# Performance work log

Measured on AMD Instinct MI355X. Metric: run time of the kernel, lower is better.

## Reference

```python
import jax, jax.numpy as jnp
import numpy as np

N_HEADS = 16
EMBED = 1024
HEAD_SIZE = 64
BLOCK = 2048
BATCH = 4


def setup_inputs() -> dict:
    key = jax.random.key(0)
    ks = jax.random.split(key, 6)
    s = 1.0 / np.sqrt(EMBED)
    X = jax.random.normal(ks[0], (BATCH, BLOCK, EMBED), dtype=jnp.float32)
    Wq = jax.random.normal(ks[1], (N_HEADS, EMBED, HEAD_SIZE), dtype=jnp.float32) * s
    Wk = jax.random.normal(ks[2], (N_HEADS, EMBED, HEAD_SIZE), dtype=jnp.float32) * s
    Wv = jax.random.normal(ks[3], (N_HEADS, EMBED, HEAD_SIZE), dtype=jnp.float32) * s
    Wo = jax.random.normal(ks[4], (EMBED, EMBED), dtype=jnp.float32) * s
    bo = jnp.zeros((EMBED,), dtype=jnp.float32)
    return {"X": X, "Wq": Wq, "Wk": Wk, "Wv": Wv, "Wo": Wo, "bo": bo}


def reference(X, Wq, Wk, Wv, Wo, bo):
    # X: [B, S, E]; Wq/Wk/Wv: [H, E, Dh]
    q = jnp.einsum("bse,hed->bhsd", X, Wq)
    k = jnp.einsum("bse,hed->bhsd", X, Wk)
    v = jnp.einsum("bse,hed->bhsd", X, Wv)
    scale = 1.0 / np.sqrt(HEAD_SIZE)
    scores = jnp.einsum("bhsd,bhtd->bhst", q, k) * scale  # [B,H,S,S]
    S = X.shape[1]
    causal = jnp.tril(jnp.ones((S, S), dtype=bool))
    scores = jnp.where(causal, scores, -jnp.inf)
    wei = jax.nn.softmax(scores, axis=-1)
    # dropout p=0.2 treated as identity (eval mode) for deterministic reference
    out = jnp.einsum("bhst,bhtd->bhsd", wei, v)  # [B,H,S,Dh]
    out = out.transpose(0, 2, 1, 3).reshape(X.shape[0], S, N_HEADS * HEAD_SIZE)
    return out @ Wo.T + bo
```

## Files before the change

kernel.cpp:

```cpp
#include <hip/hip_runtime.h>
#include <stdint.h>


typedef __bf16 bf16_t;
typedef __bf16 bf16x4 __attribute__((ext_vector_type(4)));
typedef __bf16 bf16x8 __attribute__((ext_vector_type(8)));
typedef float  f32x4  __attribute__((ext_vector_type(4)));
typedef float  f32x16 __attribute__((ext_vector_type(16)));
typedef unsigned int u32;

union V8 { bf16x8 v8; bf16x4 h[2]; u32 w[4]; };

__device__ __forceinline__ void gload_lds16(const void* g, void* l) {
  __builtin_amdgcn_global_load_lds((const __attribute__((address_space(1))) void*)g,
                                   (__attribute__((address_space(3))) void*)l, 16, 0, 0);
}


__global__ __launch_bounds__(256) void mha_prep_all(const float* __restrict__ X,
                                                    const float* __restrict__ Wq,
                                                    const float* __restrict__ Wk,
                                                    const float* __restrict__ Wv,
                                                    const float* __restrict__ Wo,
                                                    bf16_t* __restrict__ Xb,
                                                    bf16_t* __restrict__ Wob,
                                                    bf16_t* __restrict__ Wt) {
  const int bx = blockIdx.x;
  if (bx < 4608) {
    const float* src = (bx < 4096) ? X : Wo;
    bf16_t* dst = (bx < 4096) ? Xb : Wob;
    size_t base = (size_t)((bx < 4096) ? bx : bx - 4096) * 256 + threadIdx.x;
    size_t i = base * 8;
    const float4* p = (const float4*)(src + i);
    float4 a = p[0], b = p[1];
    bf16x8 o;
    o[0] = (__bf16)a.x; o[1] = (__bf16)a.y; o[2] = (__bf16)a.z; o[3] = (__bf16)a.w;
    o[4] = (__bf16)b.x; o[5] = (__bf16)b.y; o[6] = (__bf16)b.z; o[7] = (__bf16)b.w;
    *(bf16x8*)(dst + i) = o;
  } else {
    __shared__ float tile[64][65];
    const int pid = bx - 4608;
    const int e0 = (pid & 15) * 64;
    const int mh = pid >> 4;
    const int mat = mh >> 4, h = mh & 15;
    const float* W = (mat == 0) ? Wq : (mat == 1) ? Wk : Wv;
    const float sc = (mat == 0) ? 0.18033688011112042f : 1.0f;
    #pragma unroll
    for (int i = 0; i < 16; i++) {
      int idx = threadIdx.x + i * 256;
      int er = idx >> 6, d = idx & 63;
      tile[er][d] = W[(size_t)(h * 1024 + e0 + er) * 64 + d];
    }
    __syncthreads();
    #pragma unroll
    for (int i = 0; i < 16; i++) {
      int idx = threadIdx.x + i * 256;
      int dr = idx >> 6, ec = idx & 63;
      Wt[(size_t)(mat * 1024 + h * 64 + dr) * 1024 + e0 + ec] = (bf16_t)(tile[ec][dr] * sc);
    }
  }
}


__global__ __launch_bounds__(512, 2) void gemm192(const bf16_t* __restrict__ A,
                                                  const bf16_t* __restrict__ Bt,
                                                  bf16_t* __restrict__ C,
                                                  int M, int N, int K) {
  __shared__ __align__(16) char lds[131072];
  const int tid = threadIdx.x;
  const int l = tid & 63, w = tid >> 6;
  const int g = l >> 4, lg = l & 15;
  const int wr = w >> 2, wc = w & 3;
  const int bid = blockIdx.x;
  const int nbn = N / 192;
  const int gsw = (bid & 7) * (gridDim.x >> 3) + (bid >> 3);
  const long brow = (long)(gsw / nbn) * 256;
  const long bcol = (long)(gsw % nbn) * 192;

  f32x4 acc[8][3];
  #pragma unroll
  for (int im = 0; im < 8; im++)
    #pragma unroll
    for (int n = 0; n < 3; n++) acc[im][n] = (f32x4){0.f, 0.f, 0.f, 0.f};

  auto stage = [&](const bf16_t* base, long trow, int k0, int region, bool pad) {
    #pragma unroll
    for (int j = 0; j < 2; j++) {
      int p = (tid + j * 512) * 16;
      int row = p >> 6, slot = (p >> 4) & 3;
      int src = slot ^ ((row >> 1) & 3);
      int r2 = (pad && row >= 192) ? row - 192 : row;
      gload_lds16(base + (trow + r2) * (long)K + k0 + src * 8,
                  lds + region + p);
    }
  };

  stage(A,  brow, 0,  0,              false);
  stage(Bt, bcol, 0,  65536,          true);
  stage(A,  brow, 32, 16384,          false);
  stage(Bt, bcol, 32, 65536 + 16384,  true);
  stage(A,  brow, 64, 32768,          false);
  stage(Bt, bcol, 64, 65536 + 32768,  true);
  asm volatile("s_waitcnt vmcnt(4)" ::: "memory");
  __builtin_amdgcn_s_barrier();
  __builtin_amdgcn_sched_barrier(0);

  const int sw = (lg >> 1) & 3;
  const int nIter = K >> 7;
  for (int t = 0; t < nIter; t++) {
    const bool more = (t + 1 < nIter);
    const int kb = t * 128;
    #pragma unroll
    for (int ph = 0; ph < 8; ph++) {
      const int slot = ph >> 2;
      const int kh = (ph >> 1) & 1, mq = ph & 1;
      bf16x8 af[4], bfv[3];
      {
        const char* pA = lds + slot * 32768 + kh * 16384;
        const char* pB = pA + 65536;
        #pragma unroll
        for (int m = 0; m < 4; m++) {
          int wrow = wr * 128 + mq * 64 + m * 16 + lg;
          af[m] = *(const bf16x8*)(pA + wrow * 64 + ((g ^ sw) << 4));
        }
        #pragma unroll
        for (int n = 0; n < 3; n++) {
          int wrow = wc * 48 + n * 16 + lg;
          bfv[n] = *(const bf16x8*)(pB + wrow * 64 + ((g ^ sw) << 4));
        }
      }
      if (ph == 0)      stage(A,  brow, kb + 96,  32768 + 16384, false);
      else if (ph == 1) stage(Bt, bcol, kb + 96,  65536 + 32768 + 16384, true);
      else if (more) {
        if (ph == 2)      stage(A,  brow, kb + 128, 0, false);
        else if (ph == 3) stage(Bt, bcol, kb + 128, 65536, true);
        else if (ph == 4) stage(A,  brow, kb + 160, 16384, false);
        else if (ph == 5) stage(Bt, bcol, kb + 160, 65536 + 16384, true);
        else if (ph == 6) stage(A,  brow, kb + 192, 32768, false);
        else              stage(Bt, bcol, kb + 192, 65536 + 32768, true);
      }
      __builtin_amdgcn_s_barrier();
      asm volatile("s_waitcnt lgkmcnt(0)" ::: "memory");
      __builtin_amdgcn_sched_barrier(0);
      __builtin_amdgcn_s_setprio(1);
      #pragma unroll
      for (int m = 0; m < 4; m++)
        #pragma unroll
        for (int n = 0; n < 3; n++)
          acc[mq * 4 + m][n] =
              __builtin_amdgcn_mfma_f32_16x16x32_bf16(af[m], bfv[n], acc[mq * 4 + m][n], 0, 0, 0);
      __builtin_amdgcn_s_setprio(0);
      __builtin_amdgcn_sched_barrier(0);
      if (ph & 1) {
        if (more) asm volatile("s_waitcnt vmcnt(4)" ::: "memory");
        else if (ph == 1) asm volatile("s_waitcnt vmcnt(0)" ::: "memory");
      }
      __builtin_amdgcn_s_barrier();
      __builtin_amdgcn_sched_barrier(0);
    }
  }

  #pragma unroll
  for (int im = 0; im < 8; im++)
    #pragma unroll
    for (int n = 0; n < 3; n++) {
      long row0 = brow + wr * 128 + im * 16 + g * 4;
      long col  = bcol + wc * 48 + n * 16 + lg;
      #pragma unroll
      for (int r = 0; r < 4; r++)
        C[(row0 + r) * N + col] = (bf16_t)acc[im][n][r];
    }
}


template <int MODE>
__global__ __launch_bounds__(256) void gemm_bt(const bf16_t* __restrict__ A,
                                               const bf16_t* __restrict__ Bt,
                                               void* __restrict__ Cout,
                                               const float* __restrict__ bias,
                                               int M, int N, int K) {
  __shared__ bf16_t lA[128 * 32];
  __shared__ bf16_t lB[128 * 32];
  const int tid = threadIdx.x;
  const int l = tid & 63, w = tid >> 6;
  const int g = l >> 4, lg = l & 15;
  const int wr = w >> 1, wc = w & 1;
  const long brow = (long)blockIdx.y * 128;
  const long bcol = (long)blockIdx.x * 128;

  f32x4 acc[4][4];
  #pragma unroll
  for (int m = 0; m < 4; m++)
    #pragma unroll
    for (int n = 0; n < 4; n++) acc[m][n] = (f32x4){0.f, 0.f, 0.f, 0.f};

  const bf16_t* Ab = A + brow * K;
  const bf16_t* Bb = Bt + bcol * K;
  const int c0 = tid, c1 = tid + 256;
  const int r0 = c0 >> 2, o0 = (c0 & 3) * 8;
  const int r1 = c1 >> 2, o1 = (c1 & 3) * 8;

  for (int k0 = 0; k0 < K; k0 += 32) {
    __syncthreads();
    gload_lds16(Ab + (long)r0 * K + k0 + o0, lA + c0 * 8);
    gload_lds16(Ab + (long)r1 * K + k0 + o1, lA + c1 * 8);
    gload_lds16(Bb + (long)r0 * K + k0 + o0, lB + c0 * 8);
    gload_lds16(Bb + (long)r1 * K + k0 + o1, lB + c1 * 8);
    __syncthreads();
    bf16x8 af[4], bfr[4];
    #pragma unroll
    for (int m = 0; m < 4; m++)
      af[m] = *(const bf16x8*)(lA + (wr * 64 + m * 16 + lg) * 32 + g * 8);
    #pragma unroll
    for (int n = 0; n < 4; n++)
      bfr[n] = *(const bf16x8*)(lB + (wc * 64 + n * 16 + lg) * 32 + g * 8);
    #pragma unroll
    for (int m = 0; m < 4; m++)
      #pragma unroll
      for (int n = 0; n < 4; n++)
        acc[m][n] = __builtin_amdgcn_mfma_f32_16x16x32_bf16(af[m], bfr[n], acc[m][n], 0, 0, 0);
  }

  #pragma unroll
  for (int m = 0; m < 4; m++) {
    #pragma unroll
    for (int n = 0; n < 4; n++) {
      long row0 = brow + wr * 64 + m * 16 + g * 4;
      long col  = bcol + wc * 64 + n * 16 + lg;
      if (MODE == 0) {
        bf16_t* Cb = (bf16_t*)Cout;
        #pragma unroll
        for (int r = 0; r < 4; r++) Cb[(row0 + r) * N + col] = (bf16_t)acc[m][n][r];
      } else {
        float* Cf = (float*)Cout;
        float bv = bias[col];
        #pragma unroll
        for (int r = 0; r < 4; r++) Cf[(row0 + r) * N + col] = acc[m][n][r] + bv;
      }
    }
  }
}


__global__ __launch_bounds__(256, 3) void mha_attn4(const bf16_t* __restrict__ QKV,
                                                    bf16_t* __restrict__ AO) {
  __shared__ __align__(16) char smem[49152];
  const int tid = threadIdx.x;
  const int l = tid & 63, w = tid >> 6;
  const int q31 = l & 31;
  const int hi = l >> 5;
  const int hb = (l >> 4) & 1;
  const int lg = l & 15;

  const int bid = blockIdx.x;
  const int xcd = bid & 7, ii = bid >> 3;
  const int bh = xcd * 8 + (ii & 7);
  const int stripe = 15 - (ii >> 3);
  const int b = bh >> 4, h = bh & 15;

  const int qw = stripe * 128 + w * 32;
  const bf16_t* Qp = QKV + (size_t)b * 2048 * 3072 + h * 64;
  const bf16_t* Kp = Qp + 1024;
  const bf16_t* Vp = Qp + 2048;

  bf16x8 qf[4];
  {
    const bf16_t* qrow = Qp + (size_t)(qw + q31) * 3072 + hi * 8;
    #pragma unroll
    for (int ks = 0; ks < 4; ks++) qf[ks] = *(const bf16x8*)(qrow + ks * 16);
  }

  f32x16 o0, o1, z16;
  #pragma unroll
  for (int r = 0; r < 16; r++) { o0[r] = 0.f; o1[r] = 0.f; z16[r] = 0.f; }
  float lsum = 0.f;

  const int tmaxw = 2 * stripe + 1 + (w >> 1);
  const int T = 2 * stripe + 2;
  const u32 ldsbase = (u32)(uintptr_t)(__attribute__((address_space(3))) char*)smem;

  u32 vb0[2][4];
  #pragma unroll
  for (int mb = 0; mb < 2; mb++)
    #pragma unroll
    for (int ks = 0; ks < 4; ks++)
      vb0[mb][ks] = ldsbase + 24576u +
                    (u32)(((ks * 4 + 2 * mb + hb) << 9) + hi * 256 + lg * 8);

  const int krow = tid >> 3, kcb = (tid & 7) * 16;
  const int kscb = kcb ^ ((krow & 7) << 4);
  const int st0 = tid >> 5, qq0 = tid & 31;
  const int st1 = (tid + 256) >> 5;
  const bf16_t* kp0 = Kp + (size_t)krow * 3072 + (kscb >> 1);
  const bf16_t* kp1 = kp0 + (size_t)32 * 3072;
  const bf16_t* vp0 = Vp + (size_t)((st0 >> 2) * 16 + (qq0 >> 1)) * 3072 + (st0 & 3) * 16 + (qq0 & 1) * 8;
  const bf16_t* vp1 = Vp + (size_t)((st1 >> 2) * 16 + (qq0 >> 1)) * 3072 + (st1 & 3) * 16 + (qq0 & 1) * 8;
  const size_t KVSTEP = (size_t)64 * 3072;

  auto stage = [&](int bi) {
    char* kb = smem + bi * 8192;
    char* vb = smem + 24576 + bi * 8192;
    gload_lds16(kp0, kb + tid * 16);
    gload_lds16(vp0, vb + tid * 16);
    gload_lds16(kp1, kb + (tid + 256) * 16);
    gload_lds16(vp1, vb + (tid + 256) * 16);
    kp0 += KVSTEP; kp1 += KVSTEP; vp0 += KVSTEP; vp1 += KVSTEP;
  };

  stage(0);
  int cur3 = 0;
  for (int t = 0; t < T; t++) {
    int nxt3 = cur3 + 1; if (nxt3 == 3) nxt3 = 0;
    if (t + 1 < T) {
      stage(nxt3);
      __builtin_amdgcn_sched_barrier(0);
      asm volatile("s_waitcnt vmcnt(4)" ::: "memory");
    } else {
      __builtin_amdgcn_sched_barrier(0);
      asm volatile("s_waitcnt vmcnt(0)" ::: "memory");
    }
    __builtin_amdgcn_sched_barrier(0);
    __builtin_amdgcn_s_barrier();
    __builtin_amdgcn_sched_barrier(0);

    const bool active = (t < tmaxw);
    u32 paw[4][4];
    if (active) {
      f32x16 p0, p1;
      {
        const char* kb = smem + cur3 * 8192;
        const int rb0 = q31 * 128;
        const int swz = (l & 7) << 4;
        __builtin_amdgcn_s_setprio(1);
        {
          int colb = (hi << 4) ^ swz;
          bf16x8 kf0 = *(const bf16x8*)(kb + rb0 + colb);
          bf16x8 kf1 = *(const bf16x8*)(kb + 4096 + rb0 + colb);
          p0 = __builtin_amdgcn_mfma_f32_32x32x16_bf16(kf0, qf[0], z16, 0, 0, 0);
          p1 = __builtin_amdgcn_mfma_f32_32x32x16_bf16(kf1, qf[0], z16, 0, 0, 0);
        }
        #pragma unroll
        for (int ks = 1; ks < 4; ks++) {
          int colb = ((ks << 5) | (hi << 4)) ^ swz;
          bf16x8 kf0 = *(const bf16x8*)(kb + rb0 + colb);
          bf16x8 kf1 = *(const bf16x8*)(kb + 4096 + rb0 + colb);
          p0 = __builtin_amdgcn_mfma_f32_32x32x16_bf16(kf0, qf[ks], p0, 0, 0, 0);
          p1 = __builtin_amdgcn_mfma_f32_32x32x16_bf16(kf1, qf[ks], p1, 0, 0, 0);
        }
        __builtin_amdgcn_s_setprio(0);
      }
      if (t == tmaxw - 1) {
        int q = qw + q31;
        int kvb = t * 64 + 4 * hi;
        #pragma unroll
        for (int r = 0; r < 16; r++) {
          int kv0 = kvb + (r & 3) + 8 * (r >> 2);
          if (kv0 > q) p0[r] = -1e30f;
          if (kv0 + 32 > q) p1[r] = -1e30f;
        }
      }
      #pragma unroll
      for (int r = 0; r < 16; r++) p0[r] = exp2f(p0[r]);
      #pragma unroll
      for (int r = 0; r < 16; r++) p1[r] = exp2f(p1[r]);
      float s8[8];
      #pragma unroll
      for (int r = 0; r < 8; r++)
        s8[r] = (p0[r] + p0[r + 8]) + (p1[r] + p1[r + 8]);
      float rs = ((s8[0] + s8[1]) + (s8[2] + s8[3])) + ((s8[4] + s8[5]) + (s8[6] + s8[7]));
      rs += __shfl_xor(rs, 32);
      lsum += rs;
      #pragma unroll
      for (int gblk = 0; gblk < 4; gblk++) {
        int base = (gblk & 1) * 8;
        float e0 = (gblk < 2) ? p0[base + 0] : p1[base + 0];
        float e1 = (gblk < 2) ? p0[base + 1] : p1[base + 1];
        float e2 = (gblk < 2) ? p0[base + 2] : p1[base + 2];
        float e3 = (gblk < 2) ? p0[base + 3] : p1[base + 3];
        float e4 = (gblk < 2) ? p0[base + 4] : p1[base + 4];
        float e5 = (gblk < 2) ? p0[base + 5] : p1[base + 5];
        float e6 = (gblk < 2) ? p0[base + 6] : p1[base + 6];
        float e7 = (gblk < 2) ? p0[base + 7] : p1[base + 7];
        u32 u0, u1, v0, v1;
        asm("v_cvt_pk_bf16_f32 %0, %1, %2" : "=v"(u0) : "v"(e0), "v"(e1));
        asm("v_cvt_pk_bf16_f32 %0, %1, %2" : "=v"(u1) : "v"(e2), "v"(e3));
        asm("v_cvt_pk_bf16_f32 %0, %1, %2" : "=v"(v0) : "v"(e4), "v"(e5));
        asm("v_cvt_pk_bf16_f32 %0, %1, %2" : "=v"(v1) : "v"(e6), "v"(e7));
        asm("v_permlane32_swap_b32 %0, %1" : "+v"(u0), "+v"(v0));
        asm("v_permlane32_swap_b32 %0, %1" : "+v"(u1), "+v"(v1));
        paw[gblk][0] = u0; paw[gblk][1] = u1; paw[gblk][2] = v0; paw[gblk][3] = v1;
      }
      V8 vf[2][4];
      const u32 boff = (u32)cur3 * 8192u;
      #pragma unroll
      for (int mb = 0; mb < 2; mb++)
        #pragma unroll
        for (int ks = 0; ks < 4; ks++) {
          u32 base = vb0[mb][ks] + boff;
          bf16x4 t0, t1;
          asm volatile("ds_read_b64_tr_b16 %0, %1" : "=v"(t0) : "v"(base));
          asm volatile("ds_read_b64_tr_b16 %0, %1 offset:128" : "=v"(t1) : "v"(base));
          vf[mb][ks].h[0] = t0; vf[mb][ks].h[1] = t1;
        }
      asm volatile("s_waitcnt lgkmcnt(0)" ::: "memory");
      __builtin_amdgcn_sched_barrier(0);
      __builtin_amdgcn_s_setprio(1);
      #pragma unroll
      for (int ks = 0; ks < 4; ks++) {
        V8 pa; pa.w[0] = paw[ks][0]; pa.w[1] = paw[ks][1]; pa.w[2] = paw[ks][2]; pa.w[3] = paw[ks][3];
        o0 = __builtin_amdgcn_mfma_f32_32x32x16_bf16(vf[0][ks].v8, pa.v8, o0, 0, 0, 0);
        o1 = __builtin_amdgcn_mfma_f32_32x32x16_bf16(vf[1][ks].v8, pa.v8, o1, 0, 0, 0);
      }
      __builtin_amdgcn_s_setprio(0);
    }
    cur3 = nxt3;
  }

  float linv = 1.f / lsum;
  __syncthreads();
  bf16_t* ow = (bf16_t*)smem + w * 2048;
  #pragma unroll
  for (int mb = 0; mb < 2; mb++)
    #pragma unroll
    for (int r = 0; r < 16; r += 2) {
      int d = mb * 32 + (r & 3) + 8 * (r >> 2) + 4 * hi;
      float a0 = (mb ? o1[r] : o0[r]) * linv;
      float a1 = (mb ? o1[r + 1] : o0[r + 1]) * linv;
      u32 pk;
      asm("v_cvt_pk_bf16_f32 %0, %1, %2" : "=v"(pk) : "v"(a0), "v"(a1));
      int byteoff = q31 * 128 + ((d * 2) ^ ((q31 & 7) << 4));
      *(u32*)((char*)ow + byteoff) = pk;
    }
  __syncthreads();
  const size_t aorow0 = (size_t)b * 2048 + qw;
  #pragma unroll
  for (int it = 0; it < 4; it++) {
    int idx = it * 64 + l;
    int q = idx >> 3, cc = idx & 7;
    bf16x8 v8 = *(const bf16x8*)((const char*)ow + q * 128 + ((cc * 16) ^ ((q & 7) << 4)));
    *(bf16x8*)(AO + (aorow0 + q) * 1024 + h * 64 + cc * 8) = v8;
  }
}


extern "C" void kernel_launch(void* const* d_in, const int* in_sizes, int n_in,
                              void* d_out, int out_size, void* d_ws, size_t ws_size,
                              hipStream_t stream) {
  (void)in_sizes; (void)n_in; (void)out_size; (void)ws_size;
  const float* X  = (const float*)d_in[0];
  const float* Wq = (const float*)d_in[1];
  const float* Wk = (const float*)d_in[2];
  const float* Wv = (const float*)d_in[3];
  const float* Wo = (const float*)d_in[4];
  const float* bo = (const float*)d_in[5];
  float* out = (float*)d_out;

  char* ws = (char*)d_ws;
  bf16_t* Xb  = (bf16_t*)ws;
  bf16_t* AO  = Xb;
  bf16_t* Wt  = (bf16_t*)(ws + (16u << 20));
  bf16_t* Wob = (bf16_t*)(ws + (22u << 20));
  bf16_t* QKV = (bf16_t*)(ws + (24u << 20));

  mha_prep_all<<<dim3(5376), dim3(256), 0, stream>>>(X, Wq, Wk, Wv, Wo, Xb, Wob, Wt);
  gemm192<<<dim3(512), dim3(512), 0, stream>>>(Xb, Wt, QKV, 8192, 3072, 1024);
  mha_attn4<<<dim3(1024), dim3(256), 0, stream>>>(QKV, AO);
  gemm_bt<1><<<dim3(1024 / 128, 8192 / 128), dim3(256), 0, stream>>>(
      AO, Wob, (void*)out, bo, 8192, 1024, 1024);
}
```

Measured before the change: 167.7 us.

## Replace output projection GEMM with pipelined multi-stage 256x128 tile kernel

Swaps the simple single-buffered 128x128 output-projection GEMM for a 512-thread kernel with 256x128 tiles. It keeps several K-slices in flight in LDS through async global-to-LDS loads, interleaved with MFMA phases. It also adds an XOR swizzle against LDS bank conflicts and an XCD-aware block remap for better L2 locality. The goal is to hide global memory latency that the old load-sync-compute loop exposed. The cost is 128KB of LDS per block, which limits occupancy to one block per CU, plus redundant B loads into padded regions.

Result: faster. 161.2 us (-3.9%).

```diff
diff --git a/kernel.cpp b/kernel.cpp
--- a/kernel.cpp
+++ b/kernel.cpp
@@ -173,72 +173,116 @@
 }
 
 
-template <int MODE>
-__global__ __launch_bounds__(256) void gemm_bt(const bf16_t* __restrict__ A,
-                                               const bf16_t* __restrict__ Bt,
-                                               void* __restrict__ Cout,
-                                               const float* __restrict__ bias,
-                                               int M, int N, int K) {
-  __shared__ bf16_t lA[128 * 32];
-  __shared__ bf16_t lB[128 * 32];
+__global__ __launch_bounds__(512, 2) void gemm128o(const bf16_t* __restrict__ A,
+                                                   const bf16_t* __restrict__ Bt,
+                                                   float* __restrict__ C,
+                                                   const float* __restrict__ bias,
+                                                   int M, int N, int K) {
+  __shared__ __align__(16) char lds[131072];
   const int tid = threadIdx.x;
   const int l = tid & 63, w = tid >> 6;
   const int g = l >> 4, lg = l & 15;
-  const int wr = w >> 1, wc = w & 1;
-  const long brow = (long)blockIdx.y * 128;
-  const long bcol = (long)blockIdx.x * 128;
-
-  f32x4 acc[4][4];
-  #pragma unroll
-  for (int m = 0; m < 4; m++)
-    #pragma unroll
-    for (int n = 0; n < 4; n++) acc[m][n] = (f32x4){0.f, 0.f, 0.f, 0.f};
-
-  const bf16_t* Ab = A + brow * K;
-  const bf16_t* Bb = Bt + bcol * K;
-  const int c0 = tid, c1 = tid + 256;
-  const int r0 = c0 >> 2, o0 = (c0 & 3) * 8;
-  const int r1 = c1 >> 2, o1 = (c1 & 3) * 8;
-
-  for (int k0 = 0; k0 < K; k0 += 32) {
-    __syncthreads();
-    gload_lds16(Ab + (long)r0 * K + k0 + o0, lA + c0 * 8);
-    gload_lds16(Ab + (long)r1 * K + k0 + o1, lA + c1 * 8);
-    gload_lds16(Bb + (long)r0 * K + k0 + o0, lB + c0 * 8);
-    gload_lds16(Bb + (long)r1 * K + k0 + o1, lB + c1 * 8);
-    __syncthreads();
-    bf16x8 af[4], bfr[4];
-    #pragma unroll
-    for (int m = 0; m < 4; m++)
-      af[m] = *(const bf16x8*)(lA + (wr * 64 + m * 16 + lg) * 32 + g * 8);
-    #pragma unroll
-    for (int n = 0; n < 4; n++)
-      bfr[n] = *(const bf16x8*)(lB + (wc * 64 + n * 16 + lg) * 32 + g * 8);
-    #pragma unroll
-    for (int m = 0; m < 4; m++)
-      #pragma unroll
-      for (int n = 0; n < 4; n++)
-        acc[m][n] = __builtin_amdgcn_mfma_f32_16x16x32_bf16(af[m], bfr[n], acc[m][n], 0, 0, 0);
+  const int wr = w >> 2, wc = w & 3;
+  const int bid = blockIdx.x;
+  const int nbn = N >> 7;
+  const int gsw = (bid & 7) * (gridDim.x >> 3) + (bid >> 3);
+  const long brow = (long)(gsw / nbn) * 256;
+  const long bcol = (long)(gsw % nbn) * 128;
+
+  f32x4 acc[8][2];
+  #pragma unroll
+  for (int im = 0; im < 8; im++)
+    #pragma unroll
+    for (int n = 0; n < 2; n++) acc[im][n] = (f32x4){0.f, 0.f, 0.f, 0.f};
+
+  auto stage = [&](const bf16_t* base, long trow, int k0, int region, bool pad) {
+    #pragma unroll
+    for (int j = 0; j < 2; j++) {
+      int p = (tid + j * 512) * 16;
+      int row = p >> 6, slot = (p >> 4) & 3;
+      int src = slot ^ ((row >> 1) & 3);
+      int r2 = pad ? (row & 127) : row;
+      gload_lds16(base + (trow + r2) * (long)K + k0 + src * 8,
+                  lds + region + p);
+    }
+  };
+
+  stage(A,  brow, 0,  0,              false);
+  stage(Bt, bcol, 0,  65536,          true);
+  stage(A,  brow, 32, 16384,          false);
+  stage(Bt, bcol, 32, 65536 + 16384,  true);
+  stage(A,  brow, 64, 32768,          false);
+  stage(Bt, bcol, 64, 65536 + 32768,  true);
+  asm volatile("s_waitcnt vmcnt(4)" ::: "memory");
+  __builtin_amdgcn_s_barrier();
+  __builtin_amdgcn_sched_barrier(0);
+
+  const int sw = (lg >> 1) & 3;
+  const int nIter = K >> 7;
+  for (int t = 0; t < nIter; t++) {
+    const bool more = (t + 1 < nIter);
+    const int kb = t * 128;
+    #pragma unroll
+    for (int ph = 0; ph < 8; ph++) {
+      const int slot = ph >> 2;
+      const int kh = (ph >> 1) & 1, mq = ph & 1;
+      bf16x8 af[4], bfv[2];
+      {
+        const char* pA = lds + slot * 32768 + kh * 16384;
+        const char* pB = pA + 65536;
+        #pragma unroll
+        for (int m = 0; m < 4; m++) {
+          int wrow = wr * 128 + mq * 64 + m * 16 + lg;
+          af[m] = *(const bf16x8*)(pA + wrow * 64 + ((g ^ sw) << 4));
+        }
+        #pragma unroll
+        for (int n = 0; n < 2; n++) {
+          int wrow = wc * 32 + n * 16 + lg;
+          bfv[n] = *(const bf16x8*)(pB + wrow * 64 + ((g ^ sw) << 4));
+        }
+      }
+      if (ph == 0)      stage(A,  brow, kb + 96,  32768 + 16384, false);
+      else if (ph == 1) stage(Bt, bcol, kb + 96,  65536 + 32768 + 16384, true);
+      else if (more) {
+        if (ph == 2)      stage(A,  brow, kb + 128, 0, false);
+        else if (ph == 3) stage(Bt, bcol, kb + 128, 65536, true);
+        else if (ph == 4) stage(A,  brow, kb + 160, 16384, false);
+        else if (ph == 5) stage(Bt, bcol, kb + 160, 65536 + 16384, true);
+        else if (ph == 6) stage(A,  brow, kb + 192, 32768, false);
+        else              stage(Bt, bcol, kb + 192, 65536 + 32768, true);
+      }
+      __builtin_amdgcn_s_barrier();
+      asm volatile("s_waitcnt lgkmcnt(0)" ::: "memory");
+      __builtin_amdgcn_sched_barrier(0);
+      __builtin_amdgcn_s_setprio(1);
+      #pragma unroll
+      for (int m = 0; m < 4; m++)
+        #pragma unroll
+        for (int n = 0; n < 2; n++)
+          acc[mq * 4 + m][n] =
+              __builtin_amdgcn_mfma_f32_16x16x32_bf16(af[m], bfv[n], acc[mq * 4 + m][n], 0, 0, 0);
+      __builtin_amdgcn_s_setprio(0);
+      __builtin_amdgcn_sched_barrier(0);
+      if (ph & 1) {
+        if (more) asm volatile("s_waitcnt vmcnt(4)" ::: "memory");
+        else if (ph == 1) asm volatile("s_waitcnt vmcnt(0)" ::: "memory");
+      }
+      __builtin_amdgcn_s_barrier();
+      __builtin_amdgcn_sched_barrier(0);
+    }
   }
 
   #pragma unroll
-  for (int m = 0; m < 4; m++) {
-    #pragma unroll
-    for (int n = 0; n < 4; n++) {
-      long row0 = brow + wr * 64 + m * 16 + g * 4;
-      long col  = bcol + wc * 64 + n * 16 + lg;
-      if (MODE == 0) {
-        bf16_t* Cb = (bf16_t*)Cout;
-        #pragma unroll
-        for (int r = 0; r < 4; r++) Cb[(row0 + r) * N + col] = (bf16_t)acc[m][n][r];
-      } else {
-        float* Cf = (float*)Cout;
-        float bv = bias[col];
-        #pragma unroll
-        for (int r = 0; r < 4; r++) Cf[(row0 + r) * N + col] = acc[m][n][r] + bv;
-      }
-    }
-  }
+  for (int im = 0; im < 8; im++)
+    #pragma unroll
+    for (int n = 0; n < 2; n++) {
+      long row0 = brow + wr * 128 + im * 16 + g * 4;
+      long col  = bcol + wc * 32 + n * 16 + lg;
+      float bv = bias[col];
+      #pragma unroll
+      for (int r = 0; r < 4; r++)
+        C[(row0 + r) * N + col] = acc[im][n][r] + bv;
+    }
 }
 
 
@@ -465,6 +509,5 @@
   mha_prep_all<<<dim3(5376), dim3(256), 0, stream>>>(X, Wq, Wk, Wv, Wo, Xb, Wob, Wt);
   gemm192<<<dim3(512), dim3(512), 0, stream>>>(Xb, Wt, QKV, 8192, 3072, 1024);
   mha_attn4<<<dim3(1024), dim3(256), 0, stream>>>(QKV, AO);
-  gemm_bt<1><<<dim3(1024 / 128, 8192 / 128), dim3(256), 0, stream>>>(
-      AO, Wob, (void*)out, bo, 8192, 1024, 1024);
+  gemm128o<<<dim3(256), dim3(512), 0, stream>>>(AO, Wob, out, bo, 8192, 1024, 1024);
 }
```
